# Performance work log

Measured on AMD Instinct MI355X. Metric: run time of the kernel, lower is better.

## Reference

```python
import jax, jax.numpy as jnp
import numpy as np

NUM_STREAM = 4
SINKHORN_ITERS = 20
HC_EPS = 1e-06
NORM_EPS = 1e-06


def sinkhorn_knopps(h, iters, eps):
    # h: [B, S, ns, ns]
    h = jax.nn.softmax(h, axis=-1) + eps
    h = h / (h.sum(-2, keepdims=True) + eps)
    for _ in range(iters - 1):  # fixed small trip count (19), unrolled
        h = h / (h.sum(-1, keepdims=True) + eps)
        h = h / (h.sum(-2, keepdims=True) + eps)
    return h


def setup_inputs() -> dict:
    key = jax.random.key(0)
    k1, k2, k3, k4 = jax.random.split(key, 4)
    B, S, ns, H = 4, 2048, NUM_STREAM, 1024
    mix_hc = (2 + ns) * ns  # 24
    x = jax.random.normal(k1, (B, S, ns, H), dtype=jnp.float32)
    hc_fn = jax.random.normal(k2, (mix_hc, ns * H), dtype=jnp.float32) * 0.02
    hc_scale = jax.random.uniform(k3, (3,), dtype=jnp.float32)
    hc_base = jax.random.normal(k4, (mix_hc,), dtype=jnp.float32)
    return {"x": x, "hc_fn": hc_fn, "hc_scale": hc_scale, "hc_base": hc_base}


def reference(x, hc_fn, hc_scale, hc_base):
    B, S, ns, H = x.shape
    xf = x.reshape(B, S, ns * H).astype(jnp.float32)
    # RMSNorm stats (applied as a post-scale on the linear output, as in source)
    rsqrt = jax.lax.rsqrt(jnp.mean(jnp.square(xf), axis=-1, keepdims=True) + NORM_EPS)
    weight = jnp.einsum('bsd,md->bsm', xf, hc_fn) * rsqrt  # [B, S, mix_hc]
    h_pre = weight[..., :ns]
    h_post = weight[..., ns:2 * ns]
    h_res = weight[..., 2 * ns:].reshape(B, S, ns, ns)
    h_pre = jax.nn.sigmoid(h_pre * hc_scale[0] + hc_base[:ns][None, None, :]) + HC_EPS
    h_post = 2.0 * jax.nn.sigmoid(h_post * hc_scale[1] + hc_base[ns:2 * ns][None, None, :])
    h_res = h_res * hc_scale[2] + hc_base[2 * ns:].reshape(ns, ns)[None, None, :, :]
    h_res = sinkhorn_knopps(h_res, SINKHORN_ITERS, HC_EPS)
    xs = xf.reshape(B, S, ns, H)
    # hc_pre: mix streams into a single vector per token
    y = jnp.einsum('bsn,bsnh->bsh', h_pre, xs)  # [B, S, H]
    # hc_post: broadcast gated y back to streams + Sinkhorn-mixed residual streams
    out = h_post[..., None] * y[:, :, None, :] + jnp.einsum('bsij,bsih->bsjh', h_res, xs)
    return out.astype(x.dtype)
```

## Files before the change

kernel.cpp:

```cpp
#include <hip/hip_runtime.h>
#include <math.h>

#define NS 4
#define HDIM 1024
#define DDIM 4096
#define TA 4
#define HC_EPS_F 1e-6f
#define NORM_EPS_F 1e-6f

__device__ __forceinline__ float frcp(float v) { return __builtin_amdgcn_rcpf(v); }

__launch_bounds__(256, 2)
__global__ void mhc_gates(const float* __restrict__ x,
                          const float* __restrict__ hc_fn,
                          const float* __restrict__ hc_scale,
                          const float* __restrict__ hc_base,
                          float* __restrict__ gates) {
  __shared__ float w_s[25][TA];

  const int tid  = threadIdx.x;
  const int lane = tid & 63;
  const int wave = tid >> 6;
  const long long tok0 = (long long)blockIdx.x * TA;

  const float4* xb[TA];
  #pragma unroll
  for (int t = 0; t < TA; ++t)
    xb[t] = (const float4*)(x + (tok0 + t) * DDIM);

  const int mb = wave * 6;
  const float4* fn4[6];
  #pragma unroll
  for (int m = 0; m < 6; ++m)
    fn4[m] = (const float4*)(hc_fn + (long long)(mb + m) * DDIM);

  float acc[6][TA];
  #pragma unroll
  for (int m = 0; m < 6; ++m)
    #pragma unroll
    for (int t = 0; t < TA; ++t) acc[m][t] = 0.f;
  float myssq = 0.f;

  float4 c_x[TA];
  #pragma unroll
  for (int t = 0; t < TA; ++t) c_x[t] = xb[t][lane];

  #pragma unroll 2
  for (int it = 0; it < 16; ++it) {
    const int fl = it * 64 + lane;
    float4 n_x[TA];
    if (it < 15) {
      #pragma unroll
      for (int t = 0; t < TA; ++t) n_x[t] = xb[t][fl + 64];
    }
    float4 c_f[6];
    #pragma unroll
    for (int m = 0; m < 6; ++m) c_f[m] = fn4[m][fl];

    #pragma unroll
    for (int t = 0; t < TA; ++t) {
      if (wave == t)
        myssq = fmaf(c_x[t].x, c_x[t].x, fmaf(c_x[t].y, c_x[t].y,
                fmaf(c_x[t].z, c_x[t].z, fmaf(c_x[t].w, c_x[t].w, myssq))));
      #pragma unroll
      for (int m = 0; m < 6; ++m)
        acc[m][t] = fmaf(c_x[t].x, c_f[m].x,
                    fmaf(c_x[t].y, c_f[m].y,
                    fmaf(c_x[t].z, c_f[m].z,
                    fmaf(c_x[t].w, c_f[m].w, acc[m][t]))));
    }
    if (it < 15) {
      #pragma unroll
      for (int t = 0; t < TA; ++t) c_x[t] = n_x[t];
    }
  }

  #pragma unroll
  for (int m = 0; m < 6; ++m)
    #pragma unroll
    for (int t = 0; t < TA; ++t) {
      float v = acc[m][t];
      #pragma unroll
      for (int off = 32; off > 0; off >>= 1) v += __shfl_xor(v, off, 64);
      if (lane == 0) w_s[mb + m][t] = v;
    }
  {
    float v = myssq;
    #pragma unroll
    for (int off = 32; off > 0; off >>= 1) v += __shfl_xor(v, off, 64);
    if (lane == 0) w_s[24][wave] = v;
  }
  __syncthreads();

  if (wave == 0) {
    const int tt = lane >> 4;
    const int e  = lane & 15;
    const float rs = rsqrtf(w_s[24][tt] * (1.0f / DDIM) + NORM_EPS_F);
    const float s0 = hc_scale[0], s1 = hc_scale[1], s2 = hc_scale[2];

    float h = w_s[8 + e][tt] * rs * s2 + hc_base[8 + e];
    float mx = fmaxf(h, __shfl_xor(h, 1, 4));
    mx = fmaxf(mx, __shfl_xor(mx, 2, 4));
    float ex = expf(h - mx);
    float sm = ex + __shfl_xor(ex, 1, 4);
    sm += __shfl_xor(sm, 2, 4);
    h = ex * frcp(sm) + HC_EPS_F;
    float cs = h + __shfl_xor(h, 4, 16);
    cs += __shfl_xor(cs, 8, 16);
    h *= frcp(cs + HC_EPS_F);
    #pragma unroll 1
    for (int itn = 0; itn < 19; ++itn) {
      float rsum = h + __shfl_xor(h, 1, 4);
      rsum += __shfl_xor(rsum, 2, 4);
      h *= frcp(rsum + HC_EPS_F);
      float csum = h + __shfl_xor(h, 4, 16);
      csum += __shfl_xor(csum, 8, 16);
      h *= frcp(csum + HC_EPS_F);
    }
    float* g = gates + (tok0 + tt) * 24;
    g[8 + e] = h;
    if (e < NS) {
      const float wp = w_s[e][tt] * rs;
      g[e] = frcp(1.0f + expf(-(wp * s0 + hc_base[e]))) + HC_EPS_F;
      const float wq = w_s[NS + e][tt] * rs;
      g[NS + e] = 2.0f * frcp(1.0f + expf(-(wq * s1 + hc_base[NS + e])));
    }
  }
}

__launch_bounds__(256, 8)
__global__ void mhc_out(const float* __restrict__ x,
                        const float* __restrict__ gates,
                        float* __restrict__ out) {
  const long long token = blockIdx.x;
  const int q = threadIdx.x;

  const float* g = gates + token * 24;
  float hp[NS], hq[NS], hr[NS][NS];
  #pragma unroll
  for (int i = 0; i < NS; ++i) {
    hp[i] = g[i];
    hq[i] = g[NS + i];
    #pragma unroll
    for (int j = 0; j < NS; ++j) hr[i][j] = g[8 + i * NS + j];
  }

  const float4* xb = (const float4*)(x + token * DDIM);
  float4 xv[NS];
  #pragma unroll
  for (int i = 0; i < NS; ++i) xv[i] = xb[i * 256 + q];

  float4 y;
  y.x = hp[0]*xv[0].x + hp[1]*xv[1].x + hp[2]*xv[2].x + hp[3]*xv[3].x;
  y.y = hp[0]*xv[0].y + hp[1]*xv[1].y + hp[2]*xv[2].y + hp[3]*xv[3].y;
  y.z = hp[0]*xv[0].z + hp[1]*xv[1].z + hp[2]*xv[2].z + hp[3]*xv[3].z;
  y.w = hp[0]*xv[0].w + hp[1]*xv[1].w + hp[2]*xv[2].w + hp[3]*xv[3].w;

  float4* ob = (float4*)(out + token * DDIM);
  #pragma unroll
  for (int n = 0; n < NS; ++n) {
    float4 o;
    o.x = hq[n]*y.x + hr[0][n]*xv[0].x + hr[1][n]*xv[1].x + hr[2][n]*xv[2].x + hr[3][n]*xv[3].x;
    o.y = hq[n]*y.y + hr[0][n]*xv[0].y + hr[1][n]*xv[1].y + hr[2][n]*xv[2].y + hr[3][n]*xv[3].y;
    o.z = hq[n]*y.z + hr[0][n]*xv[0].z + hr[1][n]*xv[1].z + hr[2][n]*xv[2].z + hr[3][n]*xv[3].z;
    o.w = hq[n]*y.w + hr[0][n]*xv[0].w + hr[1][n]*xv[1].w + hr[2][n]*xv[2].w + hr[3][n]*xv[3].w;
    ob[n * 256 + q] = o;
  }
}

extern "C" void kernel_launch(void* const* d_in, const int* in_sizes, int n_in,
                              void* d_out, int out_size, void* d_ws, size_t ws_size,
                              hipStream_t stream) {
  const float* x        = (const float*)d_in[0];
  const float* hc_fn    = (const float*)d_in[1];
  const float* hc_scale = (const float*)d_in[2];
  const float* hc_base  = (const float*)d_in[3];
  float* out   = (float*)d_out;
  float* gates = (float*)d_ws;

  const int ntok = in_sizes[0] / DDIM;
  mhc_gates<<<ntok / TA, 256, 0, stream>>>(x, hc_fn, hc_scale, hc_base, gates);
  mhc_out<<<ntok, 256, 0, stream>>>(x, gates, out);
}
```

Measured before the change: 109.4 us.

## Compute gate projections with split-bf16 MFMA and split-K atomics

Replaces the FMA-based gate projection with a kernel that splits fp32 x and hc_fn into hi/lo bf16 parts and runs three bf16 MFMAs per tile to approximate fp32 accuracy. K is split into 8 chunks across blocks, with partial results merged by atomicAdd into zeroed buffers. The Sinkhorn and sigmoid step moves into its own small kernel. This adds two memsets, one extra launch and atomic traffic, and sq is stored temporarily in the output buffer before mhc_out overwrites it. The aim is to raise parallelism and use matrix cores for the reduction-heavy projection.

```diff
diff --git a/kernel.cpp b/kernel.cpp
--- a/kernel.cpp
+++ b/kernel.cpp
@@ -4,128 +4,138 @@
 #define NS 4
 #define HDIM 1024
 #define DDIM 4096
-#define TA 4
+#define MT 16
+#define KCH 512
 #define HC_EPS_F 1e-6f
 #define NORM_EPS_F 1e-6f
 
+typedef __attribute__((ext_vector_type(8))) short short8;
+typedef __attribute__((ext_vector_type(4))) float f32x4;
+
 __device__ __forceinline__ float frcp(float v) { return __builtin_amdgcn_rcpf(v); }
 
-__launch_bounds__(256, 2)
-__global__ void mhc_gates(const float* __restrict__ x,
-                          const float* __restrict__ hc_fn,
-                          const float* __restrict__ hc_scale,
-                          const float* __restrict__ hc_base,
-                          float* __restrict__ gates) {
-  __shared__ float w_s[25][TA];
-
-  const int tid  = threadIdx.x;
-  const int lane = tid & 63;
-  const int wave = tid >> 6;
-  const long long tok0 = (long long)blockIdx.x * TA;
-
-  const float4* xb[TA];
-  #pragma unroll
-  for (int t = 0; t < TA; ++t)
-    xb[t] = (const float4*)(x + (tok0 + t) * DDIM);
-
-  const int mb = wave * 6;
-  const float4* fn4[6];
-  #pragma unroll
-  for (int m = 0; m < 6; ++m)
-    fn4[m] = (const float4*)(hc_fn + (long long)(mb + m) * DDIM);
-
-  float acc[6][TA];
-  #pragma unroll
-  for (int m = 0; m < 6; ++m)
+#define CVT_PAIR(j, f0, f1)                                                     \
+  { unsigned p0 = __float_as_uint(f0), p1 = __float_as_uint(f1);                \
+    H.u[j] = (p1 & 0xFFFF0000u) | (p0 >> 16);                                   \
+    unsigned q0 = __float_as_uint((f0) - __uint_as_float(p0 & 0xFFFF0000u));    \
+    unsigned q1 = __float_as_uint((f1) - __uint_as_float(p1 & 0xFFFF0000u));    \
+    L.u[j] = (q1 & 0xFFFF0000u) | (q0 >> 16); }
+
+__device__ __forceinline__ void cvt_hl(const float4 a, const float4 b,
+                                       short8& hi, short8& lo) {
+  union { unsigned u[4]; short8 s; } H, L;
+  CVT_PAIR(0, a.x, a.y)
+  CVT_PAIR(1, a.z, a.w)
+  CVT_PAIR(2, b.x, b.y)
+  CVT_PAIR(3, b.z, b.w)
+  hi = H.s; lo = L.s;
+}
+
+__launch_bounds__(64, 4)
+__global__ void mhc_dots_mfma(const float* __restrict__ x,
+                              const float* __restrict__ hc_fn,
+                              float* __restrict__ w,
+                              float* __restrict__ sq) {
+  const int lane = threadIdx.x;
+  const int mt = blockIdx.x >> 3;
+  const int kc = blockIdx.x & 7;
+  const long long tok0 = (long long)mt * MT;
+  const int k0 = kc * KCH;
+
+  const int row = lane & 15;
+  const int ks  = lane >> 4;
+
+  const float4* ap = (const float4*)(x + (tok0 + row) * DDIM + k0) + ks * 2;
+  const float4* bp0 = (const float4*)(hc_fn + (long long)row * DDIM + k0) + ks * 2;
+  const int fr1c = (row < 8) ? (16 + row) : 23;
+  const float4* bp1 = (const float4*)(hc_fn + (long long)fr1c * DDIM + k0) + ks * 2;
+  const bool v1 = (row < 8);
+
+  f32x4 acc0 = {0.f, 0.f, 0.f, 0.f};
+  f32x4 acc1 = {0.f, 0.f, 0.f, 0.f};
+  float ssq = 0.f;
+  const float4 z4 = {0.f, 0.f, 0.f, 0.f};
+
+  #pragma unroll
+  for (int s = 0; s < KCH / 32; ++s) {
+    const float4 a0 = ap[s * 8];
+    const float4 a1 = ap[s * 8 + 1];
+    const float4 b00 = bp0[s * 8];
+    const float4 b01 = bp0[s * 8 + 1];
+    float4 b10 = v1 ? bp1[s * 8]     : z4;
+    float4 b11 = v1 ? bp1[s * 8 + 1] : z4;
+
+    ssq = fmaf(a0.x, a0.x, fmaf(a0.y, a0.y, fmaf(a0.z, a0.z, fmaf(a0.w, a0.w, ssq))));
+    ssq = fmaf(a1.x, a1.x, fmaf(a1.y, a1.y, fmaf(a1.z, a1.z, fmaf(a1.w, a1.w, ssq))));
+
+    short8 ahi, alo, b0hi, b0lo, b1hi, b1lo;
+    cvt_hl(a0, a1, ahi, alo);
+    cvt_hl(b00, b01, b0hi, b0lo);
+    cvt_hl(b10, b11, b1hi, b1lo);
+
+    acc0 = __builtin_amdgcn_mfma_f32_16x16x32_bf16(ahi, b0hi, acc0, 0, 0, 0);
+    acc1 = __builtin_amdgcn_mfma_f32_16x16x32_bf16(ahi, b1hi, acc1, 0, 0, 0);
+    acc0 = __builtin_amdgcn_mfma_f32_16x16x32_bf16(ahi, b0lo, acc0, 0, 0, 0);
+    acc1 = __builtin_amdgcn_mfma_f32_16x16x32_bf16(ahi, b1lo, acc1, 0, 0, 0);
+    acc0 = __builtin_amdgcn_mfma_f32_16x16x32_bf16(alo, b0hi, acc0, 0, 0, 0);
+    acc1 = __builtin_amdgcn_mfma_f32_16x16x32_bf16(alo, b1hi, acc1, 0, 0, 0);
+  }
+
+  ssq += __shfl_xor(ssq, 16, 64);
+  ssq += __shfl_xor(ssq, 32, 64);
+  if (lane < 16) atomicAdd(&sq[tok0 + lane], ssq);
+
+  const int rq = lane >> 4;
+  #pragma unroll
+  for (int r = 0; r < 4; ++r)
+    atomicAdd(&w[(tok0 + rq * 4 + r) * 24 + row], acc0[r]);
+  if (row < 8) {
     #pragma unroll
-    for (int t = 0; t < TA; ++t) acc[m][t] = 0.f;
-  float myssq = 0.f;
-
-  float4 c_x[TA];
-  #pragma unroll
-  for (int t = 0; t < TA; ++t) c_x[t] = xb[t][lane];
-
-  #pragma unroll 2
-  for (int it = 0; it < 16; ++it) {
-    const int fl = it * 64 + lane;
-    float4 n_x[TA];
-    if (it < 15) {
-      #pragma unroll
-      for (int t = 0; t < TA; ++t) n_x[t] = xb[t][fl + 64];
-    }
-    float4 c_f[6];
-    #pragma unroll
-    for (int m = 0; m < 6; ++m) c_f[m] = fn4[m][fl];
-
-    #pragma unroll
-    for (int t = 0; t < TA; ++t) {
-      if (wave == t)
-        myssq = fmaf(c_x[t].x, c_x[t].x, fmaf(c_x[t].y, c_x[t].y,
-                fmaf(c_x[t].z, c_x[t].z, fmaf(c_x[t].w, c_x[t].w, myssq))));
-      #pragma unroll
-      for (int m = 0; m < 6; ++m)
-        acc[m][t] = fmaf(c_x[t].x, c_f[m].x,
-                    fmaf(c_x[t].y, c_f[m].y,
-                    fmaf(c_x[t].z, c_f[m].z,
-                    fmaf(c_x[t].w, c_f[m].w, acc[m][t]))));
-    }
-    if (it < 15) {
-      #pragma unroll
-      for (int t = 0; t < TA; ++t) c_x[t] = n_x[t];
-    }
-  }
-
-  #pragma unroll
-  for (int m = 0; m < 6; ++m)
-    #pragma unroll
-    for (int t = 0; t < TA; ++t) {
-      float v = acc[m][t];
-      #pragma unroll
-      for (int off = 32; off > 0; off >>= 1) v += __shfl_xor(v, off, 64);
-      if (lane == 0) w_s[mb + m][t] = v;
-    }
-  {
-    float v = myssq;
-    #pragma unroll
-    for (int off = 32; off > 0; off >>= 1) v += __shfl_xor(v, off, 64);
-    if (lane == 0) w_s[24][wave] = v;
-  }
-  __syncthreads();
-
-  if (wave == 0) {
-    const int tt = lane >> 4;
-    const int e  = lane & 15;
-    const float rs = rsqrtf(w_s[24][tt] * (1.0f / DDIM) + NORM_EPS_F);
-    const float s0 = hc_scale[0], s1 = hc_scale[1], s2 = hc_scale[2];
-
-    float h = w_s[8 + e][tt] * rs * s2 + hc_base[8 + e];
-    float mx = fmaxf(h, __shfl_xor(h, 1, 4));
-    mx = fmaxf(mx, __shfl_xor(mx, 2, 4));
-    float ex = expf(h - mx);
-    float sm = ex + __shfl_xor(ex, 1, 4);
-    sm += __shfl_xor(sm, 2, 4);
-    h = ex * frcp(sm) + HC_EPS_F;
-    float cs = h + __shfl_xor(h, 4, 16);
-    cs += __shfl_xor(cs, 8, 16);
-    h *= frcp(cs + HC_EPS_F);
-    #pragma unroll 1
-    for (int itn = 0; itn < 19; ++itn) {
-      float rsum = h + __shfl_xor(h, 1, 4);
-      rsum += __shfl_xor(rsum, 2, 4);
-      h *= frcp(rsum + HC_EPS_F);
-      float csum = h + __shfl_xor(h, 4, 16);
-      csum += __shfl_xor(csum, 8, 16);
-      h *= frcp(csum + HC_EPS_F);
-    }
-    float* g = gates + (tok0 + tt) * 24;
-    g[8 + e] = h;
-    if (e < NS) {
-      const float wp = w_s[e][tt] * rs;
-      g[e] = frcp(1.0f + expf(-(wp * s0 + hc_base[e]))) + HC_EPS_F;
-      const float wq = w_s[NS + e][tt] * rs;
-      g[NS + e] = 2.0f * frcp(1.0f + expf(-(wq * s1 + hc_base[NS + e])));
-    }
-  }
+    for (int r = 0; r < 4; ++r)
+      atomicAdd(&w[(tok0 + rq * 4 + r) * 24 + 16 + row], acc1[r]);
+  }
+}
+
+__launch_bounds__(256, 4)
+__global__ void mhc_sinkhorn(float* __restrict__ w,
+                             const float* __restrict__ sq,
+                             const float* __restrict__ hc_scale,
+                             const float* __restrict__ hc_base) {
+  const int lane = threadIdx.x & 63;
+  const int wave = threadIdx.x >> 6;
+  const long long tok = (long long)blockIdx.x * 16 + wave * 4 + (lane >> 4);
+  const int e = lane & 15;
+
+  float* wt = w + tok * 24;
+  const float rs = rsqrtf(sq[tok] * (1.0f / DDIM) + NORM_EPS_F);
+  const float s0 = hc_scale[0], s1 = hc_scale[1], s2 = hc_scale[2];
+
+  float h = wt[8 + e] * rs * s2 + hc_base[8 + e];
+  float mx = fmaxf(h, __shfl_xor(h, 1, 4));
+  mx = fmaxf(mx, __shfl_xor(mx, 2, 4));
+  float ex = expf(h - mx);
+  float sm = ex + __shfl_xor(ex, 1, 4);
+  sm += __shfl_xor(sm, 2, 4);
+  h = ex * frcp(sm) + HC_EPS_F;
+  float cs = h + __shfl_xor(h, 4, 16);
+  cs += __shfl_xor(cs, 8, 16);
+  h *= frcp(cs + HC_EPS_F);
+  #pragma unroll 1
+  for (int itn = 0; itn < 19; ++itn) {
+    float rsum = h + __shfl_xor(h, 1, 4);
+    rsum += __shfl_xor(rsum, 2, 4);
+    h *= frcp(rsum + HC_EPS_F);
+    float csum = h + __shfl_xor(h, 4, 16);
+    csum += __shfl_xor(csum, 8, 16);
+    h *= frcp(csum + HC_EPS_F);
+  }
+  float gp = 0.f, gq = 0.f;
+  if (e < NS) {
+    gp = frcp(1.0f + expf(-(wt[e] * rs * s0 + hc_base[e]))) + HC_EPS_F;
+    gq = 2.0f * frcp(1.0f + expf(-(wt[NS + e] * rs * s1 + hc_base[NS + e])));
+  }
+  wt[8 + e] = h;
+  if (e < NS) { wt[e] = gp; wt[NS + e] = gq; }
 }
 
 __launch_bounds__(256, 8)
@@ -175,10 +185,16 @@
   const float* hc_fn    = (const float*)d_in[1];
   const float* hc_scale = (const float*)d_in[2];
   const float* hc_base  = (const float*)d_in[3];
-  float* out   = (float*)d_out;
-  float* gates = (float*)d_ws;
+  float* out = (float*)d_out;
 
   const int ntok = in_sizes[0] / DDIM;
-  mhc_gates<<<ntok / TA, 256, 0, stream>>>(x, hc_fn, hc_scale, hc_base, gates);
-  mhc_out<<<ntok, 256, 0, stream>>>(x, gates, out);
-}
+  float* w  = (float*)d_ws;
+  float* sq = out;
+
+  hipMemsetAsync(w, 0, (size_t)ntok * 24 * sizeof(float), stream);
+  hipMemsetAsync(sq, 0, (size_t)ntok * sizeof(float), stream);
+
+  mhc_dots_mfma<<<(ntok / MT) * 8, 64, 0, stream>>>(x, hc_fn, w, sq);
+  mhc_sinkhorn<<<ntok / 16, 256, 0, stream>>>(w, sq, hc_scale, hc_base);
+  mhc_out<<<ntok, 256, 0, stream>>>(x, w, out);
+}
```

After: 130.2 us. 19.0% more time.
